# Performance work log

Hardware: AMD Instinct MI355X
Metric: run time of the kernel (lower is better)

Reference implementation:

```python
import jax, jax.numpy as jnp
import numpy as np

D_MODEL = 1024
NUM_HEADS = 16
HEAD_DIM = D_MODEL // NUM_HEADS
THETA = 10000.0
B, S = 4, 2048


def _rope(x, pos):
    # x: [B, H, S, d], pos: [B, S] int
    half = HEAD_DIM // 2
    inv_freq = THETA ** (-(jnp.arange(half, dtype=jnp.float32) * 2.0) / HEAD_DIM)  # [half]
    ang = pos.astype(jnp.float32)[:, None, :, None] * inv_freq  # [B, 1, S, half]
    cos, sin = jnp.cos(ang), jnp.sin(ang)
    x1, x2 = x[..., 0::2], x[..., 1::2]  # interleaved pairs
    r1 = x1 * cos - x2 * sin
    r2 = x1 * sin + x2 * cos
    return jnp.stack([r1, r2], axis=-1).reshape(x.shape)


def setup_inputs() -> dict:
    key = jax.random.key(0)
    ks = jax.random.split(key, 12)
    scale = 1.0 / np.sqrt(D_MODEL)
    inp = {
        "query": jax.random.normal(ks[0], (B, S, D_MODEL), dtype=jnp.float32),
        "key": jax.random.normal(ks[1], (B, S, D_MODEL), dtype=jnp.float32),
        "value": jax.random.normal(ks[2], (B, S, D_MODEL), dtype=jnp.float32),
        "token_positions": jnp.broadcast_to(jnp.arange(S, dtype=jnp.int32), (B, S)),
        "w_q": jax.random.normal(ks[3], (D_MODEL, D_MODEL), dtype=jnp.float32) * scale,
        "b_q": jnp.zeros((D_MODEL,), dtype=jnp.float32),
        "w_k": jax.random.normal(ks[4], (D_MODEL, D_MODEL), dtype=jnp.float32) * scale,
        "b_k": jnp.zeros((D_MODEL,), dtype=jnp.float32),
        "w_v": jax.random.normal(ks[5], (D_MODEL, D_MODEL), dtype=jnp.float32) * scale,
        "b_v": jnp.zeros((D_MODEL,), dtype=jnp.float32),
        "w_o": jax.random.normal(ks[6], (D_MODEL, D_MODEL), dtype=jnp.float32) * scale,
        "b_o": jnp.zeros((D_MODEL,), dtype=jnp.float32),
    }
    return inp


def reference(query, key, value, token_positions, w_q, b_q, w_k, b_k, w_v, b_v, w_o, b_o):
    b, s, _ = query.shape
    Q = query @ w_q + b_q
    K = key @ w_k + b_k
    V = value @ w_v + b_v
    # [B, S, H, d] -> [B, H, S, d]
    Q = Q.reshape(b, s, NUM_HEADS, HEAD_DIM).transpose(0, 2, 1, 3)
    K = K.reshape(b, s, NUM_HEADS, HEAD_DIM).transpose(0, 2, 1, 3)
    V = V.reshape(b, s, NUM_HEADS, HEAD_DIM).transpose(0, 2, 1, 3)
    Q = _rope(Q, token_positions)
    K = _rope(K, token_positions)
    scores = jnp.einsum("bhqd,bhkd->bhqk", Q, K) / jnp.sqrt(jnp.float32(HEAD_DIM))
    causal = jnp.tril(jnp.ones((s, s), dtype=bool))
    scores = jnp.where(causal, scores, -jnp.inf)
    attn = jax.nn.softmax(scores, axis=-1)
    out = jnp.einsum("bhqk,bhkd->bhqd", attn, V)
    out = out.transpose(0, 2, 1, 3).reshape(b, s, D_MODEL)
    return out @ w_o + b_o
```

## Files before the change

### kernel.cpp

```cpp
#include <hip/hip_runtime.h>

typedef __bf16 bf16;
typedef __attribute__((ext_vector_type(8))) __bf16 bf16x8;
typedef __attribute__((ext_vector_type(4))) __bf16 bf16x4;
typedef __attribute__((ext_vector_type(4))) float floatx4;

#define MFMA16(a, b, c) __builtin_amdgcn_mfma_f32_16x16x32_bf16((a), (b), (c), 0, 0, 0)

#define GLL(g, l)                                                   \
  __builtin_amdgcn_global_load_lds(                                 \
      (const __attribute__((address_space(1))) void*)(g),           \
      (__attribute__((address_space(3))) void*)(l), 16, 0, 0)

static constexpr int DM = 1024;
static constexpr int SEQ = 2048;
static constexpr int BATCH = 4;
static constexpr int NH = 16;
static constexpr int HD = 64;
static constexpr int NT = DM / 64;
static constexpr float LOG2E = 1.4426950408889634f;
static constexpr float LOG2_THETA = 13.287712379549449f;
static constexpr float QSC = 0.125f * LOG2E;

__global__ __launch_bounds__(256) void convert_x(
    const float* __restrict__ q, const float* __restrict__ k,
    const float* __restrict__ v, bf16* __restrict__ qo,
    bf16* __restrict__ ko, bf16* __restrict__ vo) {
  int z = blockIdx.z;
  const float* src = (z == 0) ? q : (z == 1) ? k : v;
  bf16* dst = (z == 0) ? qo : (z == 1) ? ko : vo;
  size_t i = ((size_t)blockIdx.x * blockDim.x + threadIdx.x) * 8;
  float4 a = *(const float4*)(src + i);
  float4 b = *(const float4*)(src + i + 4);
  bf16x8 o;
  o[0] = (bf16)a.x; o[1] = (bf16)a.y; o[2] = (bf16)a.z; o[3] = (bf16)a.w;
  o[4] = (bf16)b.x; o[5] = (bf16)b.y; o[6] = (bf16)b.z; o[7] = (bf16)b.w;
  *(bf16x8*)(dst + i) = o;
}

__global__ __launch_bounds__(256) void convert_w(
    const float* __restrict__ wq, const float* __restrict__ wk,
    const float* __restrict__ wv, const float* __restrict__ wo,
    bf16* __restrict__ oq, bf16* __restrict__ ok, bf16* __restrict__ ov,
    bf16* __restrict__ oo) {
  int z = blockIdx.z;
  const float* src = (z == 0) ? wq : (z == 1) ? wk : (z == 2) ? wv : wo;
  bf16* dst = (z == 0) ? oq : (z == 1) ? ok : (z == 2) ? ov : oo;
  __shared__ __align__(16) bf16 T[64][72];
  int k0 = blockIdx.y * 64, n0 = blockIdx.x * 64;
  int tid = threadIdx.x;
  int r = tid >> 4, c4 = (tid & 15) * 4;
#pragma unroll
  for (int i = 0; i < 4; i++) {
    int kk = r + i * 16;
    float4 v = *(const float4*)(src + (size_t)(k0 + kk) * DM + n0 + c4);
    T[c4 + 0][kk] = (bf16)v.x;
    T[c4 + 1][kk] = (bf16)v.y;
    T[c4 + 2][kk] = (bf16)v.z;
    T[c4 + 3][kk] = (bf16)v.w;
  }
  __syncthreads();
#pragma unroll
  for (int i = 0; i < 4; i++) {
    int nn = r + i * 16;
    bf16x4 o = *(const bf16x4*)&T[nn][c4];
    *(bf16x4*)(dst + (size_t)(n0 + nn) * DM + k0 + c4) = o;
  }
}

__global__ __launch_bounds__(256) void rope_table(const int* __restrict__ tp,
                                                  float* __restrict__ tab) {
  int idx = blockIdx.x * 256 + threadIdx.x;
  int m = idx >> 5, i = idx & 31;
  float pos = (float)tp[m];
  float invf = exp2f(-(float)(2 * i) * (LOG2_THETA / 64.0f));
  float s, c;
  sincosf(pos * invf, &s, &c);
  tab[(size_t)idx * 2] = c;
  tab[(size_t)idx * 2 + 1] = s;
}

__device__ __forceinline__ void gemm_core(const bf16* __restrict__ X,
                                          const bf16* __restrict__ Wt,
                                          bf16* As, bf16* Bs, int m0, int n0,
                                          int tid, floatx4 acc[4][4]) {
  int lane = tid & 63, wvq = tid >> 6;
  int quad = lane >> 4, low = lane & 15;
  int wm = (wvq >> 1) * 64, wn = (wvq & 1) * 64;
  int lr8 = lane >> 3;
  int swcol = ((lane & 7) ^ lr8) * 8;
  const bf16* AgL = X + (size_t)(m0 + wvq * 8 + lr8) * DM + swcol;
  const bf16* BgL = Wt + (size_t)(n0 + wvq * 8 + lr8) * DM + swcol;
  bf16* AsW = As + wvq * 512;
  bf16* BsW = Bs + wvq * 512;
  int r3 = low & 7;

#define GQ_A(kt2, b, r)                                            \
  GLL(AgL + (size_t)(kt2) * 64 + (size_t)(r) * 64 * DM,            \
      AsW + (b) * 16384 + (r) * 4096)
#define GQ_B(kt2, b, r)                                            \
  GLL(BgL + (size_t)(kt2) * 64 + (size_t)(r) * 64 * DM,            \
      BsW + (b) * 8192 + (r) * 4096)

#pragma unroll
  for (int i = 0; i < 4; i++)
#pragma unroll
    for (int j = 0; j < 4; j++) acc[i][j] = (floatx4)0.0f;

#pragma unroll
  for (int r = 0; r < 4; r++) GQ_A(0, 0, r);
#pragma unroll
  for (int r = 0; r < 2; r++) GQ_B(0, 0, r);
#pragma unroll
  for (int r = 0; r < 4; r++) GQ_A(1, 1, r);
#pragma unroll
  for (int r = 0; r < 2; r++) GQ_B(1, 1, r);
  asm volatile("s_waitcnt vmcnt(6)" ::: "memory");
  __builtin_amdgcn_s_barrier();

  int rb = 0;
  for (int t = 0; t < NT; ++t) {
    int sb = rb + 2;
    if (sb > 2) sb -= 3;
    const bf16* Ab = As + rb * 16384;
    const bf16* Bb = Bs + rb * 8192;
    bool st = (t < NT - 2);
    bf16x8 wf[4], xf[4];
#pragma unroll
    for (int i = 0; i < 4; i++)
      wf[i] = *(const bf16x8*)&Bb[(wn + i * 16 + low) * 64 + (quad ^ r3) * 8];
#pragma unroll
    for (int j = 0; j < 4; j++)
      xf[j] = *(const bf16x8*)&Ab[(wm + j * 16 + low) * 64 + (quad ^ r3) * 8];
    if (st) {
      GQ_A(t + 2, sb, 0);
      GQ_A(t + 2, sb, 1);
      GQ_B(t + 2, sb, 0);
    }
    __builtin_amdgcn_sched_barrier(0);
    __builtin_amdgcn_s_barrier();
    asm volatile("s_waitcnt lgkmcnt(0)" ::: "memory");
    __builtin_amdgcn_sched_barrier(0);
    __builtin_amdgcn_s_setprio(1);
#pragma unroll
    for (int i = 0; i < 4; i++)
#pragma unroll
      for (int j = 0; j < 4; j++)
        acc[i][j] = MFMA16(wf[i], xf[j], acc[i][j]);
    __builtin_amdgcn_s_setprio(0);
    __builtin_amdgcn_sched_barrier(0);
    __builtin_amdgcn_s_barrier();
#pragma unroll
    for (int i = 0; i < 4; i++)
      wf[i] =
          *(const bf16x8*)&Bb[(wn + i * 16 + low) * 64 + ((4 | quad) ^ r3) * 8];
#pragma unroll
    for (int j = 0; j < 4; j++)
      xf[j] =
          *(const bf16x8*)&Ab[(wm + j * 16 + low) * 64 + ((4 | quad) ^ r3) * 8];
    if (st) {
      GQ_A(t + 2, sb, 2);
      GQ_A(t + 2, sb, 3);
      GQ_B(t + 2, sb, 1);
    }
    __builtin_amdgcn_sched_barrier(0);
    __builtin_amdgcn_s_barrier();
    asm volatile("s_waitcnt lgkmcnt(0)" ::: "memory");
    __builtin_amdgcn_sched_barrier(0);
    __builtin_amdgcn_s_setprio(1);
#pragma unroll
    for (int i = 0; i < 4; i++)
#pragma unroll
      for (int j = 0; j < 4; j++)
        acc[i][j] = MFMA16(wf[i], xf[j], acc[i][j]);
    __builtin_amdgcn_s_setprio(0);
    if (st)
      asm volatile("s_waitcnt vmcnt(6)" ::: "memory");
    else
      asm volatile("s_waitcnt vmcnt(0)" ::: "memory");
    __builtin_amdgcn_sched_barrier(0);
    __builtin_amdgcn_s_barrier();
    rb = rb + 1;
    if (rb > 2) rb -= 3;
  }
#undef GQ_A
#undef GQ_B
}

__global__ __launch_bounds__(512) void gemm_qkv(
    const bf16* __restrict__ qb, const bf16* __restrict__ kb,
    const bf16* __restrict__ vb, const bf16* __restrict__ wqt,
    const bf16* __restrict__ wkt, const bf16* __restrict__ wvt,
    const float* __restrict__ biq, const float* __restrict__ bik,
    const float* __restrict__ biv, const float* __restrict__ tab,
    bf16* __restrict__ Qr, bf16* __restrict__ Kr, bf16* __restrict__ Vr) {
  int z = blockIdx.z;
  const bf16* X = (z == 0) ? qb : (z == 1) ? kb : vb;
  const bf16* Wt = (z == 0) ? wqt : (z == 1) ? wkt : wvt;
  const float* bias = (z == 0) ? biq : (z == 1) ? bik : biv;

  __shared__ __align__(16) bf16 As[3 * 256 * 64];
  __shared__ __align__(16) bf16 Bs[3 * 128 * 64];
  int lin = blockIdx.x;
  int m0 = (lin & 31) * 256, n0 = (lin >> 5) * 128;
  int tid = threadIdx.x;

  floatx4 acc[4][4];
  gemm_core(X, Wt, As, Bs, m0, n0, tid, acc);

  int lane = tid & 63, wvq = tid >> 6;
  int quad = lane >> 4, low = lane & 15;
  int wm = (wvq >> 1) * 64, wn = (wvq & 1) * 64;

#pragma unroll
  for (int i = 0; i < 4; i++) {
    int nb = n0 + wn + i * 16 + quad * 4;
    float4 bv = *(const float4*)(bias + nb);
    int h = nb >> 6, dbase = nb & 63;
#pragma unroll
    for (int j = 0; j < 4; j++) {
      int m = m0 + wm + j * 16 + low;
      int bb = m >> 11, ss = m & 2047;
      float v0 = acc[i][j][0] + bv.x;
      float v1 = acc[i][j][1] + bv.y;
      float v2 = acc[i][j][2] + bv.z;
      float v3 = acc[i][j][3] + bv.w;
      size_t off = ((size_t)(bb * NH + h) * SEQ + ss) * HD + dbase;
      bf16x4 pk;
      if (z < 2) {
        float4 cs = *(const float4*)(tab + (size_t)m * 64 + dbase);
        float o0 = v0 * cs.x - v1 * cs.y;
        float o1 = v0 * cs.y + v1 * cs.x;
        float o2 = v2 * cs.z - v3 * cs.w;
        float o3 = v2 * cs.w + v3 * cs.z;
        if (z == 0) { o0 *= QSC; o1 *= QSC; o2 *= QSC; o3 *= QSC; }
        pk[0] = (bf16)o0; pk[1] = (bf16)o1;
        pk[2] = (bf16)o2; pk[3] = (bf16)o3;
        bf16* dst = (z == 0) ? Qr : Kr;
        *(bf16x4*)(dst + off) = pk;
      } else {
        pk[0] = (bf16)v0; pk[1] = (bf16)v1;
        pk[2] = (bf16)v2; pk[3] = (bf16)v3;
        *(bf16x4*)(Vr + off) = pk;
      }
    }
  }
}

__global__ __launch_bounds__(256) void transpose_v(const bf16* __restrict__ Vr,
                                                   bf16* __restrict__ Vt) {
  int bh = blockIdx.y;
  int s0 = blockIdx.x * 64;
  __shared__ __align__(16) bf16 T[64][72];
  int t = threadIdx.x;
  int r = t >> 2, c = (t & 3) * 16;
  const bf16* src = Vr + ((size_t)bh * SEQ + s0 + r) * HD + c;
  bf16x8 a = *(const bf16x8*)src;
  bf16x8 b = *(const bf16x8*)(src + 8);
  *(bf16x8*)&T[r][c] = a;
  *(bf16x8*)&T[r][c + 8] = b;
  __syncthreads();
  bf16* dst = Vt + ((size_t)bh * HD + r) * SEQ + s0 + c;
  bf16x8 o0, o1;
#pragma unroll
  for (int j = 0; j < 8; j++) {
    o0[j] = T[c + j][r];
    o1[j] = T[c + 8 + j][r];
  }
  *(bf16x8*)dst = o0;
  *(bf16x8*)(dst + 8) = o1;
}

__global__ __launch_bounds__(256, 3) void attn_fa(const bf16* __restrict__ Qr,
                                                  const bf16* __restrict__ Kr,
                                                  const bf16* __restrict__ Vt,
                                                  bf16* __restrict__ attn) {
  int lin = blockIdx.x;
  int bh = lin & 63, qi = 15 - (lin >> 6);
  int ntiles = 2 * qi + 2;
  int tid = threadIdx.x, lane = tid & 63, w = tid >> 6;
  int quad = lane >> 4, low = lane & 15;
  __shared__ __align__(16) bf16 Ks[2][64 * 72];
  __shared__ __align__(16) bf16 Vs[2][64 * 72];
  __shared__ __align__(16) bf16 Pl[4][16 * 72];
  const bf16* Qh = Qr + (size_t)bh * SEQ * HD;
  const bf16* Kh = Kr + (size_t)bh * SEQ * HD;
  const bf16* Vh = Vt + (size_t)bh * HD * SEQ;
  int bb = bh >> 4, h = bh & 15;
  int qrow0 = qi * 128 + w * 32;

  int sr = tid >> 2, scol = (tid & 3) * 16;
  const bf16* Kg = Kh + (size_t)sr * HD + scol;
  const bf16* Vg = Vh + (size_t)sr * SEQ + scol;
  int sl = sr * 72 + scol;

  bf16x8 ones;
#pragma unroll
  for (int j = 0; j < 8; j++) ones[j] = (bf16)1.0f;

  bf16x8 aq[2][2];
#pragma unroll
  for (int rt = 0; rt < 2; rt++)
#pragma unroll
    for (int kc = 0; kc < 2; kc++)
      aq[rt][kc] = *(const bf16x8*)(Qh + (size_t)(qrow0 + rt * 16 + low) * HD +
                                    kc * 32 + quad * 8);

  floatx4 accO[2][4];
  floatx4 lacc[2];
#pragma unroll
  for (int rt = 0; rt < 2; rt++) {
    lacc[rt] = (floatx4)0.0f;
#pragma unroll
    for (int nt = 0; nt < 4; nt++) accO[rt][nt] = (floatx4)0.0f;
  }

  {
    bf16x8 k0 = *(const bf16x8*)(Kg);
    bf16x8 k1 = *(const bf16x8*)(Kg + 8);
    bf16x8 v0 = *(const bf16x8*)(Vg);
    bf16x8 v1 = *(const bf16x8*)(Vg + 8);
    *(bf16x8*)&Ks[0][sl] = k0;
    *(bf16x8*)&Ks[0][sl + 8] = k1;
    *(bf16x8*)&Vs[0][sl] = v0;
    *(bf16x8*)&Vs[0][sl + 8] = v1;
  }
  __syncthreads();

  for (int kt = 0; kt < ntiles; kt++) {
    int cur = kt & 1;
    bf16x8 nk0, nk1, nv0, nv1;
    bool pre = (kt + 1 < ntiles);
    if (pre) {
      const bf16* kg = Kg + (size_t)(kt + 1) * (64 * HD);
      const bf16* vg = Vg + (size_t)(kt + 1) * 64;
      nk0 = *(const bf16x8*)(kg);
      nk1 = *(const bf16x8*)(kg + 8);
      nv0 = *(const bf16x8*)(vg);
      nv1 = *(const bf16x8*)(vg + 8);
    }

    floatx4 s2[2][4];
#pragma unroll
    for (int rt = 0; rt < 2; rt++)
#pragma unroll
      for (int nt = 0; nt < 4; nt++) s2[rt][nt] = (floatx4)0.0f;
#pragma unroll
    for (int nt = 0; nt < 4; nt++) {
      bf16x8 kb0 = *(const bf16x8*)&Ks[cur][(nt * 16 + low) * 72 + quad * 8];
      bf16x8 kb1 =
          *(const bf16x8*)&Ks[cur][(nt * 16 + low) * 72 + 32 + quad * 8];
#pragma unroll
      for (int rt = 0; rt < 2; rt++) {
        s2[rt][nt] = MFMA16(kb0, aq[rt][0], s2[rt][nt]);
        s2[rt][nt] = MFMA16(kb1, aq[rt][1], s2[rt][nt]);
      }
    }
    if (kt >= ntiles - 2) {
#pragma unroll
      for (int nt = 0; nt < 4; nt++)
#pragma unroll
        for (int r = 0; r < 4; r++) {
          int kg_ = kt * 64 + nt * 16 + quad * 4 + r;
#pragma unroll
          for (int rt = 0; rt < 2; rt++) {
            int qg = qrow0 + rt * 16 + low;
            if (kg_ > qg) s2[rt][nt][r] = -INFINITY;
          }
        }
    }
    bf16x4 pk[2][4];
#pragma unroll
    for (int rt = 0; rt < 2; rt++)
#pragma unroll
      for (int nt = 0; nt < 4; nt++)
#pragma unroll
        for (int r = 0; r < 4; r++)
          pk[rt][nt][r] = (bf16)exp2f(s2[rt][nt][r]);
    bf16x8 vb0[4], vb1[4];
#pragma unroll
    for (int nt = 0; nt < 4; nt++) {
      vb0[nt] = *(const bf16x8*)&Vs[cur][(nt * 16 + low) * 72 + quad * 8];
      vb1[nt] = *(const bf16x8*)&Vs[cur][(nt * 16 + low) * 72 + 32 + quad * 8];
    }
#pragma unroll
    for (int rt = 0; rt < 2; rt++) {
#pragma unroll
      for (int nt = 0; nt < 4; nt++)
        *(bf16x4*)&Pl[w][low * 72 + nt * 16 + quad * 4] = pk[rt][nt];
      asm volatile("s_waitcnt lgkmcnt(0)" ::: "memory");
      bf16x8 ap0 = *(const bf16x8*)&Pl[w][low * 72 + quad * 8];
      bf16x8 ap1 = *(const bf16x8*)&Pl[w][low * 72 + 32 + quad * 8];
#pragma unroll
      for (int nt = 0; nt < 4; nt++) {
        accO[rt][nt] = MFMA16(ap0, vb0[nt], accO[rt][nt]);
        accO[rt][nt] = MFMA16(ap1, vb1[nt], accO[rt][nt]);
      }
      lacc[rt] = MFMA16(ap0, ones, lacc[rt]);
      lacc[rt] = MFMA16(ap1, ones, lacc[rt]);
    }
    if (pre) {
      int nb = cur ^ 1;
      *(bf16x8*)&Ks[nb][sl] = nk0;
      *(bf16x8*)&Ks[nb][sl + 8] = nk1;
      *(bf16x8*)&Vs[nb][sl] = nv0;
      *(bf16x8*)&Vs[nb][sl + 8] = nv1;
    }
    __syncthreads();
  }

#pragma unroll
  for (int rt = 0; rt < 2; rt++)
#pragma unroll
    for (int r = 0; r < 4; r++) {
      float inv = 1.0f / lacc[rt][r];
      int q = qrow0 + rt * 16 + quad * 4 + r;
#pragma unroll
      for (int nt = 0; nt < 4; nt++) {
        float o = accO[rt][nt][r] * inv;
        attn[((size_t)(bb * SEQ + q)) * DM + h * HD + nt * 16 + low] = (bf16)o;
      }
    }
}

__global__ __launch_bounds__(512) void gemm_out(const bf16* __restrict__ X,
                                                const bf16* __restrict__ Wt,
                                                const float* __restrict__ bias,
                                                float* __restrict__ out) {
  __shared__ __align__(16) bf16 As[3 * 256 * 64];
  __shared__ __align__(16) bf16 Bs[3 * 128 * 64];
  int lin = blockIdx.x;
  int m0 = (lin & 31) * 256, n0 = (lin >> 5) * 128;
  int tid = threadIdx.x;

  floatx4 acc[4][4];
  gemm_core(X, Wt, As, Bs, m0, n0, tid, acc);

  int lane = tid & 63, wvq = tid >> 6;
  int quad = lane >> 4, low = lane & 15;
  int wm = (wvq >> 1) * 64, wn = (wvq & 1) * 64;

#pragma unroll
  for (int i = 0; i < 4; i++) {
    int nb = n0 + wn + i * 16 + quad * 4;
    float4 bv = *(const float4*)(bias + nb);
#pragma unroll
    for (int j = 0; j < 4; j++) {
      int m = m0 + wm + j * 16 + low;
      float4 o;
      o.x = acc[i][j][0] + bv.x;
      o.y = acc[i][j][1] + bv.y;
      o.z = acc[i][j][2] + bv.z;
      o.w = acc[i][j][3] + bv.w;
      *(float4*)(out + (size_t)m * DM + nb) = o;
    }
  }
}

extern "C" void kernel_launch(void* const* d_in, const int* in_sizes, int n_in,
                              void* d_out, int out_size, void* d_ws,
                              size_t ws_size, hipStream_t stream) {
  const float* query = (const float*)d_in[0];
  const float* key_ = (const float*)d_in[1];
  const float* value = (const float*)d_in[2];
  const int* tp = (const int*)d_in[3];
  const float* w_q = (const float*)d_in[4];
  const float* b_q = (const float*)d_in[5];
  const float* w_k = (const float*)d_in[6];
  const float* b_k = (const float*)d_in[7];
  const float* w_v = (const float*)d_in[8];
  const float* b_v = (const float*)d_in[9];
  const float* w_o = (const float*)d_in[10];
  const float* b_o = (const float*)d_in[11];

  char* w = (char*)d_ws;
  const size_t MB = 1u << 20;
  bf16* qb = (bf16*)(w + 0);
  bf16* kb = (bf16*)(w + 16 * MB);
  bf16* vb = (bf16*)(w + 32 * MB);
  bf16* wqt = (bf16*)(w + 48 * MB);
  bf16* wkt = (bf16*)(w + 50 * MB);
  bf16* wvt = (bf16*)(w + 52 * MB);
  bf16* wot = (bf16*)(w + 54 * MB);
  bf16* Qr = (bf16*)(w + 56 * MB);
  bf16* Kr = (bf16*)(w + 72 * MB);
  bf16* Vr = (bf16*)(w + 88 * MB);
  float* tab = (float*)(w + 104 * MB);
  bf16* Vt = (bf16*)(w + 32 * MB);
  bf16* attnb = (bf16*)(w + 0);

  convert_x<<<dim3(4096, 1, 3), 256, 0, stream>>>(query, key_, value, qb, kb,
                                                  vb);
  convert_w<<<dim3(16, 16, 4), 256, 0, stream>>>(w_q, w_k, w_v, w_o, wqt, wkt,
                                                 wvt, wot);
  rope_table<<<1024, 256, 0, stream>>>(tp, tab);
  gemm_qkv<<<dim3(256, 1, 3), 512, 0, stream>>>(qb, kb, vb, wqt, wkt, wvt,
                                                b_q, b_k, b_v, tab, Qr, Kr,
                                                Vr);
  transpose_v<<<dim3(32, 64), 256, 0, stream>>>(Vr, Vt);
  attn_fa<<<dim3(1024), 256, 0, stream>>>(Qr, Kr, Vt, attnb);
  gemm_out<<<dim3(256), 512, 0, stream>>>(attnb, wot, b_o, (float*)d_out);
}
```

Before: 330.1 us.

## Double-buffer LDS fragment registers to overlap ds_reads with MFMA in GEMM mainloop

Restructures the GEMM K-loop so fragments for the next half-tile are read from LDS into a second register set while MFMAs run on the current set. This cuts the number of workgroup barriers per iteration from four to one and retunes the vmcnt waits to fit the new order. It is meant to hide LDS read latency behind matrix math and reduce barrier stalls. In exchange it uses more VGPRs, and the changed synchronisation around the triple-buffered global-to-LDS loads risks race conditions if the wait counts are off.

```diff
diff --git a/kernel.cpp b/kernel.cpp
--- a/kernel.cpp
+++ b/kernel.cpp
@@ -107,6 +107,27 @@
 #pragma unroll
     for (int j = 0; j < 4; j++) acc[i][j] = (floatx4)0.0f;
 
+  bf16x8 wfA[4], xfA[4], wfB[4], xfB[4];
+
+  auto ldfrag = [&](bf16x8 wf_[4], bf16x8 xf_[4], const bf16* Ab_,
+                    const bf16* Bb_, int kkb) {
+#pragma unroll
+    for (int i = 0; i < 4; i++)
+      wf_[i] = *(const bf16x8*)&Bb_[(wn + i * 16 + low) * 64 +
+                                    (((kkb << 2) | quad) ^ r3) * 8];
+#pragma unroll
+    for (int j = 0; j < 4; j++)
+      xf_[j] = *(const bf16x8*)&Ab_[(wm + j * 16 + low) * 64 +
+                                    (((kkb << 2) | quad) ^ r3) * 8];
+  };
+
+#define MFMACL(wf_, xf_)                                    \
+  __builtin_amdgcn_s_setprio(1);                            \
+  _Pragma("unroll") for (int i_ = 0; i_ < 4; i_++)          \
+      _Pragma("unroll") for (int j_ = 0; j_ < 4; j_++)      \
+          acc[i_][j_] = MFMA16(wf_[i_], xf_[j_], acc[i_][j_]); \
+  __builtin_amdgcn_s_setprio(0);
+
 #pragma unroll
   for (int r = 0; r < 4; r++) GQ_A(0, 0, r);
 #pragma unroll
@@ -117,74 +138,53 @@
   for (int r = 0; r < 2; r++) GQ_B(1, 1, r);
   asm volatile("s_waitcnt vmcnt(6)" ::: "memory");
   __builtin_amdgcn_s_barrier();
+  ldfrag(wfA, xfA, As, Bs, 0);
 
   int rb = 0;
   for (int t = 0; t < NT; ++t) {
+    int nbuf = rb + 1;
+    if (nbuf > 2) nbuf -= 3;
     int sb = rb + 2;
     if (sb > 2) sb -= 3;
     const bf16* Ab = As + rb * 16384;
     const bf16* Bb = Bs + rb * 8192;
+    const bf16* An = As + nbuf * 16384;
+    const bf16* Bn = Bs + nbuf * 8192;
     bool st = (t < NT - 2);
-    bf16x8 wf[4], xf[4];
-#pragma unroll
-    for (int i = 0; i < 4; i++)
-      wf[i] = *(const bf16x8*)&Bb[(wn + i * 16 + low) * 64 + (quad ^ r3) * 8];
-#pragma unroll
-    for (int j = 0; j < 4; j++)
-      xf[j] = *(const bf16x8*)&Ab[(wm + j * 16 + low) * 64 + (quad ^ r3) * 8];
+
+    asm volatile("s_waitcnt lgkmcnt(0)" ::: "memory");
+    __builtin_amdgcn_sched_barrier(0);
     if (st) {
       GQ_A(t + 2, sb, 0);
       GQ_A(t + 2, sb, 1);
       GQ_B(t + 2, sb, 0);
     }
+    ldfrag(wfB, xfB, Ab, Bb, 1);
     __builtin_amdgcn_sched_barrier(0);
-    __builtin_amdgcn_s_barrier();
+    MFMACL(wfA, xfA);
+    __builtin_amdgcn_sched_barrier(0);
+
     asm volatile("s_waitcnt lgkmcnt(0)" ::: "memory");
     __builtin_amdgcn_sched_barrier(0);
-    __builtin_amdgcn_s_setprio(1);
-#pragma unroll
-    for (int i = 0; i < 4; i++)
-#pragma unroll
-      for (int j = 0; j < 4; j++)
-        acc[i][j] = MFMA16(wf[i], xf[j], acc[i][j]);
-    __builtin_amdgcn_s_setprio(0);
-    __builtin_amdgcn_sched_barrier(0);
+    if (t < NT - 2)
+      asm volatile("s_waitcnt vmcnt(3)" ::: "memory");
+    else if (t == NT - 2)
+      asm volatile("s_waitcnt vmcnt(0)" ::: "memory");
     __builtin_amdgcn_s_barrier();
-#pragma unroll
-    for (int i = 0; i < 4; i++)
-      wf[i] =
-          *(const bf16x8*)&Bb[(wn + i * 16 + low) * 64 + ((4 | quad) ^ r3) * 8];
-#pragma unroll
-    for (int j = 0; j < 4; j++)
-      xf[j] =
-          *(const bf16x8*)&Ab[(wm + j * 16 + low) * 64 + ((4 | quad) ^ r3) * 8];
     if (st) {
       GQ_A(t + 2, sb, 2);
       GQ_A(t + 2, sb, 3);
       GQ_B(t + 2, sb, 1);
     }
+    if (t < NT - 1) ldfrag(wfA, xfA, An, Bn, 0);
     __builtin_amdgcn_sched_barrier(0);
-    __builtin_amdgcn_s_barrier();
-    asm volatile("s_waitcnt lgkmcnt(0)" ::: "memory");
+    MFMACL(wfB, xfB);
     __builtin_amdgcn_sched_barrier(0);
-    __builtin_amdgcn_s_setprio(1);
-#pragma unroll
-    for (int i = 0; i < 4; i++)
-#pragma unroll
-      for (int j = 0; j < 4; j++)
-        acc[i][j] = MFMA16(wf[i], xf[j], acc[i][j]);
-    __builtin_amdgcn_s_setprio(0);
-    if (st)
-      asm volatile("s_waitcnt vmcnt(6)" ::: "memory");
-    else
-      asm volatile("s_waitcnt vmcnt(0)" ::: "memory");
-    __builtin_amdgcn_sched_barrier(0);
-    __builtin_amdgcn_s_barrier();
-    rb = rb + 1;
-    if (rb > 2) rb -= 3;
+    rb = nbuf;
   }
 #undef GQ_A
 #undef GQ_B
+#undef MFMACL
 }
 
 __global__ __launch_bounds__(512) void gemm_qkv(
```

After: 348.4 us. +5.5%, slower.
